# Performance work log

Hardware: AMD Instinct MI355X
Metric: run time of the kernel (lower is better)

## Reference

```python
import jax, jax.numpy as jnp
import numpy as np

D_MODEL = 1024
NUM_HEADS = 16
D_K = D_MODEL // NUM_HEADS
B, S = 4, 2048
NEG = -1e9


def setup_inputs() -> dict:
    key = jax.random.key(0)
    ks = jax.random.split(key, 12)
    def lin(kw, kb):
        bound = 1.0 / np.sqrt(D_MODEL)
        W = jax.random.uniform(kw, (D_MODEL, D_MODEL), jnp.float32, -bound, bound)
        b = jax.random.uniform(kb, (D_MODEL,), jnp.float32, -bound, bound)
        return W, b
    Wq, bq = lin(ks[0], ks[1])
    Wk, bk = lin(ks[2], ks[3])
    Wv, bv = lin(ks[4], ks[5])
    Wo, bo = lin(ks[6], ks[7])
    Q = jax.random.normal(ks[8], (B, S, D_MODEL), jnp.float32)
    K = jax.random.normal(ks[9], (B, S, D_MODEL), jnp.float32)
    V = jax.random.normal(ks[10], (B, S, D_MODEL), jnp.float32)
    # causal mask: 1 = keep, 0 = masked
    mask = jnp.tril(jnp.ones((S, S), jnp.int32))[None, None, :, :]
    mask = jnp.broadcast_to(mask, (B, 1, S, S))
    return {"Q": Q, "K": K, "V": V, "mask": mask,
            "Wq": Wq, "bq": bq, "Wk": Wk, "bk": bk,
            "Wv": Wv, "bv": bv, "Wo": Wo, "bo": bo}


def _split_heads(x):
    b, s, _ = x.shape
    return x.reshape(b, s, NUM_HEADS, D_K).transpose(0, 2, 1, 3)  # [B,H,S,Dk]


def reference(Q, K, V, mask, Wq, bq, Wk, bk, Wv, bv, Wo, bo):
    q = _split_heads(Q @ Wq.T + bq)
    k = _split_heads(K @ Wk.T + bk)
    v = _split_heads(V @ Wv.T + bv)
    scores = jnp.einsum('bhqd,bhkd->bhqk', q, k) / jnp.sqrt(jnp.float32(D_K))
    scores = jnp.where(mask == 0, jnp.float32(NEG), scores)
    probs = jax.nn.softmax(scores, axis=-1)
    attn = jnp.einsum('bhqk,bhkd->bhqd', probs, v)  # [B,H,S,Dk]
    attn = attn.transpose(0, 2, 1, 3).reshape(Q.shape[0], Q.shape[1], D_MODEL)
    return attn @ Wo.T + bo
```

## Files before the change

### kernel.cpp

```cpp
#include <hip/hip_runtime.h>
#include <hip/hip_bf16.h>
#include <cstdint>

typedef float floatx4 __attribute__((ext_vector_type(4)));
typedef __bf16 bf16x8 __attribute__((ext_vector_type(8)));

#define AS_G __attribute__((address_space(1)))
#define AS_L __attribute__((address_space(3)))

__device__ __forceinline__ void async_cp16(const void* g, void* l) {
    __builtin_amdgcn_global_load_lds((const AS_G uint32_t*)g, (AS_L uint32_t*)l, 16, 0, 0);
}

__device__ __forceinline__ floatx4 mfma16x16x32(bf16x8 a, bf16x8 b, floatx4 c) {
    return __builtin_amdgcn_mfma_f32_16x16x32_bf16(a, b, c, 0, 0, 0);
}

__device__ __forceinline__ unsigned short f2bf(float x) {
    return __builtin_bit_cast(unsigned short, (__bf16)x);
}

__global__ __launch_bounds__(256) void cvt4_f32_bf16(const float* __restrict__ a, const float* __restrict__ b,
                                                     const float* __restrict__ c, const float* __restrict__ d,
                                                     unsigned short* __restrict__ out, int n) {
    const float* in = blockIdx.y == 0 ? a : blockIdx.y == 1 ? b : blockIdx.y == 2 ? c : d;
    unsigned short* o = out + (size_t)blockIdx.y * n;
    int i = (blockIdx.x * 256 + threadIdx.x) * 4;
    if (i >= n) return;
    float4 v = *(const float4*)(in + i);
    ushort4 u;
    u.x = f2bf(v.x); u.y = f2bf(v.y); u.z = f2bf(v.z); u.w = f2bf(v.w);
    *(ushort4*)(o + i) = u;
}

__global__ __launch_bounds__(256) void gemm_proj(
    const float* __restrict__ Qf, const float* __restrict__ Kf, const float* __restrict__ Vf,
    const unsigned short* __restrict__ wball,
    const float* __restrict__ bq, const float* __restrict__ bk, const float* __restrict__ bv,
    float qscl,
    unsigned short* __restrict__ qp, unsigned short* __restrict__ kp,
    unsigned short* __restrict__ vtp) {
    __shared__ unsigned short As[128 * 64];
    __shared__ unsigned short Bs[128 * 64];
    const int z = blockIdx.z;
    const float* A = z == 0 ? Qf : z == 1 ? Kf : Vf;
    const unsigned short* W = wball + (size_t)z * (1024 * 1024);
    const float* bias = z == 0 ? bq : z == 1 ? bk : bv;
    const float oscale = z == 0 ? qscl : 1.0f;
    unsigned short* outp = z == 0 ? qp : z == 1 ? kp : vtp;

    const int tid  = threadIdx.x;
    const int wave = tid >> 6, lane = tid & 63;
    const int quad = lane >> 4, l15 = lane & 15;
    const int l7   = l15 & 7;
    const int m0 = blockIdx.x * 128, n0 = blockIdx.y * 128;
    const int waveM = (wave >> 1) * 64, waveN = (wave & 1) * 64;

    floatx4 acc[4][4] = {};

    const int r8  = lane >> 3;
    const int gl  = lane & 7;
    const int aphys = gl ^ r8;

    const float* Abase = A + (size_t)(m0 + wave * 32 + r8) * 1024 + gl * 8;
    float4 pa[4][2];
#pragma unroll
    for (int s = 0; s < 4; ++s) {
        const float* p = Abase + (size_t)s * 8 * 1024;
        pa[s][0] = *(const float4*)p;
        pa[s][1] = *(const float4*)(p + 4);
    }

    for (int k0 = 0; k0 < 1024; k0 += 64) {
        for (int c = wave; c < 16; c += 4) {
            const int row = c * 8 + r8;
            async_cp16(W + (size_t)(n0 + row) * 1024 + k0 + (gl ^ r8) * 8, (char*)Bs + c * 1024);
        }
#pragma unroll
        for (int s = 0; s < 4; ++s) {
            const int row = wave * 32 + s * 8 + r8;
            bf16x8 v;
            v[0] = (__bf16)pa[s][0].x; v[1] = (__bf16)pa[s][0].y;
            v[2] = (__bf16)pa[s][0].z; v[3] = (__bf16)pa[s][0].w;
            v[4] = (__bf16)pa[s][1].x; v[5] = (__bf16)pa[s][1].y;
            v[6] = (__bf16)pa[s][1].z; v[7] = (__bf16)pa[s][1].w;
            *(bf16x8*)&As[row * 64 + aphys * 8] = v;
        }
        __syncthreads();

        if (k0 + 64 < 1024) {
#pragma unroll
            for (int s = 0; s < 4; ++s) {
                const float* p = Abase + (size_t)s * 8 * 1024 + (k0 + 64);
                pa[s][0] = *(const float4*)p;
                pa[s][1] = *(const float4*)(p + 4);
            }
        }

#pragma unroll
        for (int h = 0; h < 2; ++h) {
            const int g = (quad + h * 4) ^ l7;
            bf16x8 af[4], bf[4];
#pragma unroll
            for (int t = 0; t < 4; ++t) {
                af[t] = *(const bf16x8*)&As[(waveM + t * 16 + l15) * 64 + g * 8];
                bf[t] = *(const bf16x8*)&Bs[(waveN + t * 16 + l15) * 64 + g * 8];
            }
#pragma unroll
            for (int mt = 0; mt < 4; ++mt)
#pragma unroll
                for (int nt = 0; nt < 4; ++nt)
                    acc[mt][nt] = mfma16x16x32(af[mt], bf[nt], acc[mt][nt]);
        }
        __syncthreads();
    }

#pragma unroll
    for (int mt = 0; mt < 4; ++mt) {
#pragma unroll
        for (int nt = 0; nt < 4; ++nt) {
            const int gcol = n0 + waveN + nt * 16 + l15;
            const float bv2 = bias[gcol];
#pragma unroll
            for (int r = 0; r < 4; ++r) {
                const int grow = m0 + waveM + mt * 16 + quad * 4 + r;
                const float val = (acc[mt][nt][r] + bv2) * oscale;
                const int b = grow >> 11, s = grow & 2047;
                const int h = gcol >> 6, dk = gcol & 63;
                size_t idx;
                if (z != 2) idx = ((size_t)(b * 16 + h) * 2048 + s) * 64 + dk;
                else        idx = ((size_t)(b * 16 + h) * 64 + dk) * 2048 + s;
                outp[idx] = f2bf(val);
            }
        }
    }
}

__global__ __launch_bounds__(256) void gemm_out(const unsigned short* __restrict__ A,
                                                const unsigned short* __restrict__ W,
                                                const float* __restrict__ bias,
                                                float* __restrict__ out) {
    __shared__ unsigned short As[64 * 64];
    __shared__ unsigned short Bs[128 * 64];
    const int tid  = threadIdx.x;
    const int wave = tid >> 6, lane = tid & 63;
    const int quad = lane >> 4, l15 = lane & 15;
    const int l7   = l15 & 15 & 7;
    const int m0 = blockIdx.x * 64, n0 = blockIdx.y * 128;
    const int waveM = (wave >> 1) * 32, waveN = (wave & 1) * 64;

    floatx4 acc[2][4] = {};

    const int r8  = lane >> 3;
    const int gsw = (lane & 7) ^ r8;

    for (int k0 = 0; k0 < 1024; k0 += 64) {
        for (int c = wave; c < 24; c += 4) {
            if (c < 8) {
                const int row = c * 8 + r8;
                async_cp16(A + (size_t)(m0 + row) * 1024 + k0 + gsw * 8, (char*)As + c * 1024);
            } else {
                const int row = (c - 8) * 8 + r8;
                async_cp16(W + (size_t)(n0 + row) * 1024 + k0 + gsw * 8, (char*)Bs + (c - 8) * 1024);
            }
        }
        __syncthreads();

#pragma unroll
        for (int h = 0; h < 2; ++h) {
            const int g = (quad + h * 4) ^ l7;
            bf16x8 af[2], bf[4];
#pragma unroll
            for (int t = 0; t < 2; ++t)
                af[t] = *(const bf16x8*)&As[(waveM + t * 16 + l15) * 64 + g * 8];
#pragma unroll
            for (int t = 0; t < 4; ++t)
                bf[t] = *(const bf16x8*)&Bs[(waveN + t * 16 + l15) * 64 + g * 8];
#pragma unroll
            for (int mt = 0; mt < 2; ++mt)
#pragma unroll
                for (int nt = 0; nt < 4; ++nt)
                    acc[mt][nt] = mfma16x16x32(af[mt], bf[nt], acc[mt][nt]);
        }
        __syncthreads();
    }

#pragma unroll
    for (int mt = 0; mt < 2; ++mt) {
#pragma unroll
        for (int nt = 0; nt < 4; ++nt) {
            const int gcol = n0 + waveN + nt * 16 + l15;
            const float bv = bias[gcol];
#pragma unroll
            for (int r = 0; r < 4; ++r) {
                const int grow = m0 + waveM + mt * 16 + quad * 4 + r;
                out[(size_t)grow * 1024 + gcol] = acc[mt][nt][r] + bv;
            }
        }
    }
}

#define PS_STRIDE 72

template <bool DIAG>
__device__ __forceinline__ void attn_tile(const unsigned short* __restrict__ Ks,
                                          const unsigned short* __restrict__ Vs,
                                          unsigned short* __restrict__ Psw,
                                          bf16x8 qf0, bf16x8 qf1,
                                          int quad, int l15,
                                          int qrow0,
                                          int kv0,
                                          float* __restrict__ lsum,
                                          floatx4* __restrict__ O) {
    const int l7 = l15 & 7;
    const int g1 = quad ^ l7, g2 = (quad + 4) ^ l7;

    floatx4 sc[4];
#pragma unroll
    for (int kvt = 0; kvt < 4; ++kvt) {
        const int rr = kvt * 16 + l15;
        floatx4 a = {};
        a = mfma16x16x32(qf0, *(const bf16x8*)&Ks[rr * 64 + g1 * 8], a);
        a = mfma16x16x32(qf1, *(const bf16x8*)&Ks[rr * 64 + g2 * 8], a);
        sc[kvt] = a;
    }

#pragma unroll
    for (int kvt = 0; kvt < 4; ++kvt) {
#pragma unroll
        for (int r = 0; r < 4; ++r) {
            float s = sc[kvt][r];
            if (DIAG && (kv0 + kvt * 16 + l15 > qrow0 + r)) s = -1.0e9f;
            const float p = __builtin_amdgcn_exp2f(s);
            lsum[r] += p;
            Psw[(quad * 4 + r) * PS_STRIDE + kvt * 16 + l15] = f2bf(p);
        }
    }

#pragma unroll
    for (int half = 0; half < 2; ++half) {
        bf16x8 pf = *(const bf16x8*)&Psw[l15 * PS_STRIDE + half * 32 + quad * 8];
        const int gb = (quad + half * 4) ^ l7;
#pragma unroll
        for (int nt = 0; nt < 4; ++nt) {
            bf16x8 vf = *(const bf16x8*)&Vs[(nt * 16 + l15) * 64 + gb * 8];
            O[nt] = mfma16x16x32(pf, vf, O[nt]);
        }
    }
}

__global__ __launch_bounds__(256) void flash_causal(const unsigned short* __restrict__ qp,
                                                    const unsigned short* __restrict__ kp,
                                                    const unsigned short* __restrict__ vt,
                                                    unsigned short* __restrict__ attn) {
    __shared__ unsigned short Ks[64 * 64];
    __shared__ unsigned short Vs[64 * 64];
    __shared__ unsigned short Ps[4 * 16 * PS_STRIDE];

    const int tid  = threadIdx.x;
    const int wave = tid >> 6, lane = tid & 63;
    const int quad = lane >> 4, l15 = lane & 15;
    const int bh = blockIdx.x;
    const int pr = blockIdx.y;
    const int tA = pr, tB = 31 - pr;

    unsigned short* Psw = &Ps[wave * 16 * PS_STRIDE];

    bf16x8 qfA0, qfA1, qfB0, qfB1;
    {
        const unsigned short* qa = qp + ((size_t)bh * 2048 + tA * 64 + wave * 16 + l15) * 64;
        qfA0 = *(const bf16x8*)(qa + quad * 8);
        qfA1 = *(const bf16x8*)(qa + 32 + quad * 8);
        const unsigned short* qb = qp + ((size_t)bh * 2048 + tB * 64 + wave * 16 + l15) * 64;
        qfB0 = *(const bf16x8*)(qb + quad * 8);
        qfB1 = *(const bf16x8*)(qb + 32 + quad * 8);
    }

    float lsumA[4] = {}, lsumB[4] = {};
    floatx4 OA[4] = {}, OB[4] = {};

    const int qrowA = tA * 64 + wave * 16 + quad * 4;
    const int qrowB = tB * 64 + wave * 16 + quad * 4;

    const int r8  = lane >> 3;
    const int gsw = (lane & 7) ^ r8;

    for (int t = 0; t <= tB; ++t) {
        const int kv0 = t * 64;
        for (int c = wave; c < 8; c += 4) {
            const int row = c * 8 + r8;
            async_cp16(kp + (size_t)bh * 131072 + (size_t)(kv0 + row) * 64 + gsw * 8,
                       (char*)Ks + c * 1024);
            async_cp16(vt + ((size_t)bh * 64 + row) * 2048 + kv0 + gsw * 8,
                       (char*)Vs + c * 1024);
        }
        __syncthreads();

        if (t == tB) attn_tile<true >(Ks, Vs, Psw, qfB0, qfB1, quad, l15, qrowB, kv0, lsumB, OB);
        else         attn_tile<false>(Ks, Vs, Psw, qfB0, qfB1, quad, l15, qrowB, kv0, lsumB, OB);
        if (t == tA)      attn_tile<true >(Ks, Vs, Psw, qfA0, qfA1, quad, l15, qrowA, kv0, lsumA, OA);
        else if (t < tA)  attn_tile<false>(Ks, Vs, Psw, qfA0, qfA1, quad, l15, qrowA, kv0, lsumA, OA);
        __syncthreads();
    }

    const int b = bh >> 4, h = bh & 15;
#pragma unroll
    for (int r = 0; r < 4; ++r) {
        float lA = lsumA[r], lB = lsumB[r];
#pragma unroll
        for (int off = 8; off; off >>= 1) {
            lA += __shfl_xor(lA, off, 16);
            lB += __shfl_xor(lB, off, 16);
        }
        const float invA = 1.0f / lA;
        const float invB = 1.0f / lB;
        const size_t rbA = ((size_t)b * 2048 + qrowA + r) * 1024 + h * 64;
        const size_t rbB = ((size_t)b * 2048 + qrowB + r) * 1024 + h * 64;
#pragma unroll
        for (int nt = 0; nt < 4; ++nt) {
            attn[rbA + nt * 16 + l15] = f2bf(OA[nt][r] * invA);
            attn[rbB + nt * 16 + l15] = f2bf(OB[nt][r] * invB);
        }
    }
}

extern "C" void kernel_launch(void* const* d_in, const int* in_sizes, int n_in,
                              void* d_out, int out_size, void* d_ws, size_t ws_size,
                              hipStream_t stream) {
    const float* Q  = (const float*)d_in[0];
    const float* K  = (const float*)d_in[1];
    const float* V  = (const float*)d_in[2];
    const float* Wq = (const float*)d_in[4];  const float* bq = (const float*)d_in[5];
    const float* Wk = (const float*)d_in[6];  const float* bk = (const float*)d_in[7];
    const float* Wv = (const float*)d_in[8];  const float* bv = (const float*)d_in[9];
    const float* Wo = (const float*)d_in[10]; const float* bo = (const float*)d_in[11];
    float* out = (float*)d_out;

    const int NIN = 8192 * 1024;
    const int NW  = 1024 * 1024;

    unsigned short* ws   = (unsigned short*)d_ws;
    unsigned short* wb   = ws;
    unsigned short* qp   = wb + 4 * NW;
    unsigned short* kp   = qp + NIN;
    unsigned short* vtp  = kp + NIN;
    unsigned short* attnb = vtp + NIN;

    const float QSCL = 0.125f * 1.44269504088896f;

    dim3 blk(256);
    dim3 gcvtW((NW + 1023) / 1024, 4);
    dim3 gproj(64, 8, 3);
    dim3 gout(128, 8);
    dim3 gflash(64, 16);

    cvt4_f32_bf16<<<gcvtW, blk, 0, stream>>>(Wq, Wk, Wv, Wo, wb, NW);

    gemm_proj<<<gproj, blk, 0, stream>>>(Q, K, V, wb, bq, bk, bv, QSCL, qp, kp, vtp);

    flash_causal<<<gflash, blk, 0, stream>>>(qp, kp, vtp, attnb);

    gemm_out<<<gout, blk, 0, stream>>>(attnb, wb + 3 * NW, bo, out);
}
```

Baseline: 378.5 us.

## Double-buffer LDS in projection and output GEMMs with manual waitcnt pipelining

Both GEMM kernels now use two LDS buffers so the next K-tile's global loads (async LDS copies for weights, register prefetch for fp32 activations) overlap the current tile's MFMA work. Explicit vmcnt waits and raw barriers replace __syncthreads. The output GEMM tile also grows from 64x128 to 128x128, halving its grid. The cost is doubled LDS use, which may lower occupancy, plus fragile hand-counted waitcnt values.

```diff
diff --git a/kernel.cpp b/kernel.cpp
--- a/kernel.cpp
+++ b/kernel.cpp
@@ -18,6 +18,11 @@
 
 __device__ __forceinline__ unsigned short f2bf(float x) {
     return __builtin_bit_cast(unsigned short, (__bf16)x);
+}
+
+template <int VM>
+__device__ __forceinline__ void s_wait_vm_lgkm0() {
+    __builtin_amdgcn_s_waitcnt((VM & 15) | ((VM >> 4) << 14) | (7 << 4));
 }
 
 __global__ __launch_bounds__(256) void cvt4_f32_bf16(const float* __restrict__ a, const float* __restrict__ b,
@@ -40,8 +45,8 @@
     float qscl,
     unsigned short* __restrict__ qp, unsigned short* __restrict__ kp,
     unsigned short* __restrict__ vtp) {
-    __shared__ unsigned short As[128 * 64];
-    __shared__ unsigned short Bs[128 * 64];
+    __shared__ unsigned short As[2][128 * 64];
+    __shared__ unsigned short Bs[2][128 * 64];
     const int z = blockIdx.z;
     const float* A = z == 0 ? Qf : z == 1 ? Kf : Vf;
     const unsigned short* W = wball + (size_t)z * (1024 * 1024);
@@ -55,65 +60,77 @@
     const int l7   = l15 & 7;
     const int m0 = blockIdx.x * 128, n0 = blockIdx.y * 128;
     const int waveM = (wave >> 1) * 64, waveN = (wave & 1) * 64;
+    const int r8 = lane >> 3, gl = lane & 7;
+    const int gsw = gl ^ r8;
 
     floatx4 acc[4][4] = {};
-
-    const int r8  = lane >> 3;
-    const int gl  = lane & 7;
-    const int aphys = gl ^ r8;
+    float4 pa[4][2];
 
     const float* Abase = A + (size_t)(m0 + wave * 32 + r8) * 1024 + gl * 8;
-    float4 pa[4][2];
-#pragma unroll
-    for (int s = 0; s < 4; ++s) {
-        const float* p = Abase + (size_t)s * 8 * 1024;
-        pa[s][0] = *(const float4*)p;
-        pa[s][1] = *(const float4*)(p + 4);
-    }
-
-    for (int k0 = 0; k0 < 1024; k0 += 64) {
-        for (int c = wave; c < 16; c += 4) {
-            const int row = c * 8 + r8;
-            async_cp16(W + (size_t)(n0 + row) * 1024 + k0 + (gl ^ r8) * 8, (char*)Bs + c * 1024);
-        }
-#pragma unroll
-        for (int s = 0; s < 4; ++s) {
-            const int row = wave * 32 + s * 8 + r8;
-            bf16x8 v;
-            v[0] = (__bf16)pa[s][0].x; v[1] = (__bf16)pa[s][0].y;
-            v[2] = (__bf16)pa[s][0].z; v[3] = (__bf16)pa[s][0].w;
-            v[4] = (__bf16)pa[s][1].x; v[5] = (__bf16)pa[s][1].y;
-            v[6] = (__bf16)pa[s][1].z; v[7] = (__bf16)pa[s][1].w;
-            *(bf16x8*)&As[row * 64 + aphys * 8] = v;
-        }
-        __syncthreads();
-
-        if (k0 + 64 < 1024) {
-#pragma unroll
-            for (int s = 0; s < 4; ++s) {
-                const float* p = Abase + (size_t)s * 8 * 1024 + (k0 + 64);
-                pa[s][0] = *(const float4*)p;
-                pa[s][1] = *(const float4*)(p + 4);
-            }
-        }
+
+#define LOAD_A(K)                                                    \
+    {                                                                \
+        _Pragma("unroll")                                            \
+        for (int s = 0; s < 4; ++s) {                                \
+            const float* p_ = Abase + (size_t)s * 8 * 1024 + (K);    \
+            pa[s][0] = *(const float4*)p_;                           \
+            pa[s][1] = *(const float4*)(p_ + 4);                     \
+        }                                                            \
+    }
+#define WRITE_A(DST)                                                 \
+    {                                                                \
+        _Pragma("unroll")                                            \
+        for (int s = 0; s < 4; ++s) {                                \
+            const int row_ = wave * 32 + s * 8 + r8;                 \
+            bf16x8 v_;                                               \
+            v_[0] = (__bf16)pa[s][0].x; v_[1] = (__bf16)pa[s][0].y;  \
+            v_[2] = (__bf16)pa[s][0].z; v_[3] = (__bf16)pa[s][0].w;  \
+            v_[4] = (__bf16)pa[s][1].x; v_[5] = (__bf16)pa[s][1].y;  \
+            v_[6] = (__bf16)pa[s][1].z; v_[7] = (__bf16)pa[s][1].w;  \
+            *(bf16x8*)&(DST)[row_ * 64 + gsw * 8] = v_;              \
+        }                                                            \
+    }
+#define STAGE_B(K, DST)                                              \
+    for (int c = wave; c < 16; c += 4)                               \
+        async_cp16(W + (size_t)(n0 + c * 8 + r8) * 1024 + (K) + gsw * 8, (char*)(DST) + c * 1024);
+
+    STAGE_B(0, Bs[0]);
+    LOAD_A(0);
+    WRITE_A(As[0]);
+    LOAD_A(64);
+
+    for (int k = 0; k < 16; ++k) {
+        const int p = k & 1, nb = p ^ 1;
+        __builtin_amdgcn_s_barrier();
+        if (k + 1 < 16) {
+            STAGE_B((k + 1) * 64, Bs[nb]);
+            WRITE_A(As[nb]);
+        }
+        if (k + 2 < 16) LOAD_A((k + 2) * 64);
+        if (k + 2 < 16)      s_wait_vm_lgkm0<12>();
+        else if (k + 1 < 16) s_wait_vm_lgkm0<4>();
+        else                 s_wait_vm_lgkm0<0>();
+        __builtin_amdgcn_s_barrier();
 
 #pragma unroll
         for (int h = 0; h < 2; ++h) {
             const int g = (quad + h * 4) ^ l7;
-            bf16x8 af[4], bf[4];
+            bf16x8 af[4], bfr[4];
 #pragma unroll
             for (int t = 0; t < 4; ++t) {
-                af[t] = *(const bf16x8*)&As[(waveM + t * 16 + l15) * 64 + g * 8];
-                bf[t] = *(const bf16x8*)&Bs[(waveN + t * 16 + l15) * 64 + g * 8];
+                af[t]  = *(const bf16x8*)&As[p][(waveM + t * 16 + l15) * 64 + g * 8];
+                bfr[t] = *(const bf16x8*)&Bs[p][(waveN + t * 16 + l15) * 64 + g * 8];
             }
 #pragma unroll
             for (int mt = 0; mt < 4; ++mt)
 #pragma unroll
                 for (int nt = 0; nt < 4; ++nt)
-                    acc[mt][nt] = mfma16x16x32(af[mt], bf[nt], acc[mt][nt]);
-        }
-        __syncthreads();
-    }
+                    acc[mt][nt] = mfma16x16x32(af[mt], bfr[nt], acc[mt][nt]);
+        }
+    }
+#undef LOAD_A
+#undef WRITE_A
+#undef STAGE_B
 
 #pragma unroll
     for (int mt = 0; mt < 4; ++mt) {
@@ -140,53 +157,57 @@
                                                 const unsigned short* __restrict__ W,
                                                 const float* __restrict__ bias,
                                                 float* __restrict__ out) {
-    __shared__ unsigned short As[64 * 64];
-    __shared__ unsigned short Bs[128 * 64];
+    __shared__ unsigned short As[2][128 * 64];
+    __shared__ unsigned short Bs[2][128 * 64];
     const int tid  = threadIdx.x;
     const int wave = tid >> 6, lane = tid & 63;
     const int quad = lane >> 4, l15 = lane & 15;
-    const int l7   = l15 & 15 & 7;
-    const int m0 = blockIdx.x * 64, n0 = blockIdx.y * 128;
-    const int waveM = (wave >> 1) * 32, waveN = (wave & 1) * 64;
-
-    floatx4 acc[2][4] = {};
-
-    const int r8  = lane >> 3;
+    const int l7   = l15 & 7;
+    const int m0 = blockIdx.x * 128, n0 = blockIdx.y * 128;
+    const int waveM = (wave >> 1) * 64, waveN = (wave & 1) * 64;
+    const int r8 = lane >> 3;
     const int gsw = (lane & 7) ^ r8;
 
-    for (int k0 = 0; k0 < 1024; k0 += 64) {
-        for (int c = wave; c < 24; c += 4) {
-            if (c < 8) {
-                const int row = c * 8 + r8;
-                async_cp16(A + (size_t)(m0 + row) * 1024 + k0 + gsw * 8, (char*)As + c * 1024);
-            } else {
-                const int row = (c - 8) * 8 + r8;
-                async_cp16(W + (size_t)(n0 + row) * 1024 + k0 + gsw * 8, (char*)Bs + (c - 8) * 1024);
-            }
-        }
-        __syncthreads();
+    floatx4 acc[4][4] = {};
+
+#define STAGE_AB(K, BUF)                                                                  \
+    for (int c = wave; c < 32; c += 4) {                                                  \
+        if (c < 16) async_cp16(A + (size_t)(m0 + c * 8 + r8) * 1024 + (K) + gsw * 8,      \
+                               (char*)As[BUF] + c * 1024);                                \
+        else        async_cp16(W + (size_t)(n0 + (c - 16) * 8 + r8) * 1024 + (K) + gsw * 8,\
+                               (char*)Bs[BUF] + (c - 16) * 1024);                         \
+    }
+
+    STAGE_AB(0, 0);
+
+    for (int k = 0; k < 16; ++k) {
+        const int p = k & 1, nb = p ^ 1;
+        __builtin_amdgcn_s_barrier();
+        if (k + 1 < 16) STAGE_AB((k + 1) * 64, nb);
+        if (k + 1 < 16) s_wait_vm_lgkm0<8>();
+        else            s_wait_vm_lgkm0<0>();
+        __builtin_amdgcn_s_barrier();
 
 #pragma unroll
         for (int h = 0; h < 2; ++h) {
             const int g = (quad + h * 4) ^ l7;
-            bf16x8 af[2], bf[4];
-#pragma unroll
-            for (int t = 0; t < 2; ++t)
-                af[t] = *(const bf16x8*)&As[(waveM + t * 16 + l15) * 64 + g * 8];
-#pragma unroll
-            for (int t = 0; t < 4; ++t)
-                bf[t] = *(const bf16x8*)&Bs[(waveN + t * 16 + l15) * 64 + g * 8];
-#pragma unroll
-            for (int mt = 0; mt < 2; ++mt)
+            bf16x8 af[4], bfr[4];
+#pragma unroll
+            for (int t = 0; t < 4; ++t) {
+                af[t]  = *(const bf16x8*)&As[p][(waveM + t * 16 + l15) * 64 + g * 8];
+                bfr[t] = *(const bf16x8*)&Bs[p][(waveN + t * 16 + l15) * 64 + g * 8];
+            }
+#pragma unroll
+            for (int mt = 0; mt < 4; ++mt)
 #pragma unroll
                 for (int nt = 0; nt < 4; ++nt)
-                    acc[mt][nt] = mfma16x16x32(af[mt], bf[nt], acc[mt][nt]);
-        }
-        __syncthreads();
-    }
-
-#pragma unroll
-    for (int mt = 0; mt < 2; ++mt) {
+                    acc[mt][nt] = mfma16x16x32(af[mt], bfr[nt], acc[mt][nt]);
+        }
+    }
+#undef STAGE_AB
+
+#pragma unroll
+    for (int mt = 0; mt < 4; ++mt) {
 #pragma unroll
         for (int nt = 0; nt < 4; ++nt) {
             const int gcol = n0 + waveN + nt * 16 + l15;
@@ -351,7 +372,7 @@
     dim3 blk(256);
     dim3 gcvtW((NW + 1023) / 1024, 4);
     dim3 gproj(64, 8, 3);
-    dim3 gout(128, 8);
+    dim3 gout(64, 8);
     dim3 gflash(64, 16);
 
     cvt4_f32_bf16<<<gcvtW, blk, 0, stream>>>(Wq, Wk, Wv, Wo, wb, NW);
```

Measured after the change: 373.9 us. No clear change (-1.2%).
